# Optimization experiments

Hardware: AMD Instinct MI355X
Metric: run time of the kernel (lower is better)

Reference implementation:

```python
import jax, jax.numpy as jnp
import numpy as np
import math

B, S, D, H, N = 4, 2048, 1024, 8, 128  # batch, seq_len, d_model, n_heads, num_osc
ITERS = 10
DT = 0.1
PI = math.pi


def setup_inputs() -> dict:
    key = jax.random.key(0)
    ks = jax.random.split(key, 5)
    return {
        "x": jax.random.normal(ks[0], (B, S, D), jnp.float32),
        "mask": jnp.ones((B, S), jnp.int32),
        "W_phase": jax.random.normal(ks[1], (D, H * N), jnp.float32) / math.sqrt(D),
        "b_phase": jnp.zeros((H * N,), jnp.float32),
        "natural_freq": jax.random.normal(ks[2], (H, N), jnp.float32) * 0.1,
        "coupling": jnp.ones((H, 1, 1), jnp.float32),  # coupling_strength = 1.0
        "W_out": jax.random.normal(ks[3], (H * N, D), jnp.float32) / math.sqrt(H * N),
        "b_out": jnp.zeros((D,), jnp.float32),
    }


def reference(x, mask, W_phase, b_phase, natural_freq, coupling, W_out, b_out):
    # phases: [B, H, S, N]
    ph = (x @ W_phase + b_phase).reshape(B, S, H, N).transpose(0, 2, 1, 3)
    ph = jnp.tanh(ph) * PI
    m = mask.astype(ph.dtype)[:, None, :, None]  # [B,1,S,1] mask over j
    K = coupling.reshape(1, H, 1, 1)
    w = natural_freq.reshape(1, H, 1, N)

    def step(ph, _):
        s = jnp.sin(ph)
        c = jnp.cos(ph)
        # mean_j m_j * sin(theta_i - theta_j) = sin(th_i)*mean(m*cos) - cos(th_i)*mean(m*sin)
        ms = (m * s).mean(axis=2, keepdims=True)  # [B,H,1,N]
        mc = (m * c).mean(axis=2, keepdims=True)
        dtheta = w + K * (s * mc - c * ms)
        ph2 = jnp.mod(ph + DT * dtheta + PI, 2 * PI) - PI
        return ph2, None

    ph, _ = jax.lax.scan(step, ph, None, length=ITERS)
    # from_phase; dropout is identity in eval mode
    y = ph.transpose(0, 2, 1, 3).reshape(B, S, H * N) @ W_out + b_out
    return y
```

## Files before the change

### kernel.cpp

```cpp
#include <hip/hip_runtime.h>
#include <math.h>

#define S_ 2048
#define D_ 1024
#define HN_ 1024
#define B_ 4
#define M_ 8192
#define K1_ 3072
#define K3_ 1024
#define ITERS_ 10
#define DT_ 0.1f
#define PI_ 3.14159265358979323846f
#define TWOPI_ 6.28318530717958647692f
#define INV2PI_ 0.15915494309189533577f
#define SCALE_ 4096.0f
#define INVSC2_ (1.0f / 16777216.0f)

typedef __attribute__((ext_vector_type(8))) _Float16 f16x8;
typedef __attribute__((ext_vector_type(4))) float f32x4;

__device__ ushort g_xs [(size_t)M_ * K1_];
__device__ ushort g_WpT[(size_t)HN_ * K1_];
__device__ float  g_ph [(size_t)B_ * HN_ * S_];
__device__ ushort g_phh[(size_t)B_ * HN_ * S_];
__device__ ushort g_phT[(size_t)M_ * HN_];
__device__ ushort g_WoT[(size_t)D_ * HN_];

__device__ __forceinline__ ushort f2h(float f) {
    union { _Float16 h; ushort u; } v; v.h = (_Float16)f; return v.u;
}
__device__ __forceinline__ void split2s(float x, ushort& A, ushort& Bc) {
    const float xs = x * SCALE_;
    union { _Float16 h; ushort u; } va, vb;
    va.h = (_Float16)xs;
    const float r = xs - (float)va.h;
    vb.h = (_Float16)r;
    A = va.u; Bc = vb.u;
}
__device__ __forceinline__ void gload16(const void* g, void* l) {
    __builtin_amdgcn_global_load_lds(
        (const __attribute__((address_space(1))) void*)g,
        (__attribute__((address_space(3))) void*)l, 16, 0, 0);
}
__device__ __forceinline__ int pack2(ushort a, ushort b) {
    return (int)(unsigned)a | ((int)(unsigned)b << 16);
}

__global__ __launch_bounds__(256) void split_x(const float* __restrict__ X) {
    const int idx = blockIdx.x * 256 + threadIdx.x;
    const float4 v = ((const float4*)X)[idx];
    const int m  = idx >> 8;
    const int k4 = (idx & 255) * 4;
    ushort a[4], b[4];
    split2s(v.x, a[0], b[0]);
    split2s(v.y, a[1], b[1]);
    split2s(v.z, a[2], b[2]);
    split2s(v.w, a[3], b[3]);
    ushort* row = g_xs + (size_t)m * K1_ + k4;
    int2 oa; oa.x = pack2(a[0], a[1]); oa.y = pack2(a[2], a[3]);
    int2 ob; ob.x = pack2(b[0], b[1]); ob.y = pack2(b[2], b[3]);
    *(int2*)(row)        = oa;
    *(int2*)(row + 1024) = oa;
    *(int2*)(row + 2048) = ob;
}

__global__ __launch_bounds__(256) void splitT_Wp(const float* __restrict__ Wp) {
    __shared__ float t[64][68];
    const int k0 = blockIdx.x * 64;
    const int n0 = blockIdx.y * 64;
    const int r = threadIdx.x >> 2;
    const int c = (threadIdx.x & 3) * 16;
    const float* src = Wp + (size_t)(k0 + r) * HN_ + n0 + c;
    #pragma unroll
    for (int q = 0; q < 4; ++q)
        *(float4*)&t[r][c + 4 * q] = ((const float4*)src)[q];
    __syncthreads();
    ushort ha[16], hb[16];
    #pragma unroll
    for (int j = 0; j < 16; ++j)
        split2s(t[c + j][r], ha[j], hb[j]);
    int4 a0, a1, b0, b1;
    a0.x = pack2(ha[0], ha[1]);   a0.y = pack2(ha[2], ha[3]);
    a0.z = pack2(ha[4], ha[5]);   a0.w = pack2(ha[6], ha[7]);
    a1.x = pack2(ha[8], ha[9]);   a1.y = pack2(ha[10], ha[11]);
    a1.z = pack2(ha[12], ha[13]); a1.w = pack2(ha[14], ha[15]);
    b0.x = pack2(hb[0], hb[1]);   b0.y = pack2(hb[2], hb[3]);
    b0.z = pack2(hb[4], hb[5]);   b0.w = pack2(hb[6], hb[7]);
    b1.x = pack2(hb[8], hb[9]);   b1.y = pack2(hb[10], hb[11]);
    b1.z = pack2(hb[12], hb[13]); b1.w = pack2(hb[14], hb[15]);
    ushort* dst = g_WpT + (size_t)(n0 + r) * K1_ + k0 + c;
    *(int4*)(dst)            = a0; *(int4*)(dst + 8)        = a1;
    *(int4*)(dst + 1024)     = b0; *(int4*)(dst + 1032)     = b1;
    *(int4*)(dst + 2048)     = a0; *(int4*)(dst + 2056)     = a1;
}

__global__ __launch_bounds__(256) void castT_Wo(const float* __restrict__ Wo) {
    __shared__ float t[64][68];
    const int k0 = blockIdx.x * 64;
    const int n0 = blockIdx.y * 64;
    const int r = threadIdx.x >> 2;
    const int c = (threadIdx.x & 3) * 16;
    const float* src = Wo + (size_t)(k0 + r) * D_ + n0 + c;
    #pragma unroll
    for (int q = 0; q < 4; ++q)
        *(float4*)&t[r][c + 4 * q] = ((const float4*)src)[q];
    __syncthreads();
    ushort h[16];
    #pragma unroll
    for (int j = 0; j < 16; ++j) h[j] = f2h(t[c + j][r]);
    ushort* dst = g_WoT + (size_t)(n0 + r) * HN_ + k0 + c;
    int4 o0, o1;
    o0.x = pack2(h[0], h[1]);   o0.y = pack2(h[2], h[3]);
    o0.z = pack2(h[4], h[5]);   o0.w = pack2(h[6], h[7]);
    o1.x = pack2(h[8], h[9]);   o1.y = pack2(h[10], h[11]);
    o1.z = pack2(h[12], h[13]); o1.w = pack2(h[14], h[15]);
    *(int4*)dst = o0;
    *(int4*)(dst + 8) = o1;
}

template<int KDIM>
__device__ __forceinline__ void gemm_mainloop(const ushort* __restrict__ A,
                                              const ushort* __restrict__ Bm,
                                              ushort* lds,
                                              int m0, int n0, int wid, int l,
                                              int wm, int wn,
                                              f32x4 (&acc)[4][4]) {
    constexpr int NT = KDIM / 64;
    const int r8   = l >> 3;
    const int swzo = ((l & 7) * 16) ^ (r8 << 4);
    const char* gA = (const char*)(A + (size_t)m0 * KDIM);
    const char* gB = (const char*)(Bm + (size_t)n0 * KDIM);

    const int thr = (l & 15) * 128;
    const int f0  = (((l >> 4) * 16)      ^ ((l & 7) << 4));
    const int f1  = ((64 + (l >> 4) * 16) ^ ((l & 7) << 4));
    const char* pA0 = (const char*)lds + wm * 8192 + thr + f0;
    const char* pA1 = (const char*)lds + wm * 8192 + thr + f1;
    const char* pB0 = (const char*)lds + 16384 + wn * 8192 + thr + f0;
    const char* pB1 = (const char*)lds + 16384 + wn * 8192 + thr + f1;

    #define STAGE(T, BUF) do {                                                    \
        const size_t gb_ = (size_t)(T) * 128 + swzo;                              \
        char* lb_ = (char*)lds + (BUF) * 32768 + wid * 1024;                      \
        _Pragma("unroll")                                                         \
        for (int j_ = 0; j_ < 4; ++j_)                                            \
            gload16(gA + (size_t)(j_ * 32 + wid * 8 + r8) * (KDIM * 2) + gb_,     \
                    lb_ + j_ * 4096);                                             \
        _Pragma("unroll")                                                         \
        for (int j_ = 0; j_ < 4; ++j_)                                            \
            gload16(gB + (size_t)(j_ * 32 + wid * 8 + r8) * (KDIM * 2) + gb_,     \
                    lb_ + 16384 + j_ * 4096);                                     \
    } while (0)

    STAGE(0, 0);

    #pragma unroll 2
    for (int t = 0; t < NT; ++t) {
        __builtin_amdgcn_sched_barrier(0);
        __builtin_amdgcn_s_barrier();
        __builtin_amdgcn_sched_barrier(0);
        if (t + 1 < NT) {
            STAGE(t + 1, (t + 1) & 1);
            asm volatile("s_waitcnt vmcnt(8)" ::: "memory");
        } else {
            asm volatile("s_waitcnt vmcnt(0)" ::: "memory");
        }
        __builtin_amdgcn_sched_barrier(0);
        __builtin_amdgcn_s_barrier();
        __builtin_amdgcn_sched_barrier(0);

        const int bo = (t & 1) << 15;
        f16x8 Aa[4][2], Bb[4][2];
        #pragma unroll
        for (int i = 0; i < 4; ++i) {
            Aa[i][0] = *(const f16x8*)(pA0 + bo + i * 2048);
            Aa[i][1] = *(const f16x8*)(pA1 + bo + i * 2048);
        }
        #pragma unroll
        for (int j = 0; j < 4; ++j) {
            Bb[j][0] = *(const f16x8*)(pB0 + bo + j * 2048);
            Bb[j][1] = *(const f16x8*)(pB1 + bo + j * 2048);
        }
        __builtin_amdgcn_s_setprio(1);
        #pragma unroll
        for (int ks = 0; ks < 2; ++ks)
            #pragma unroll
            for (int i = 0; i < 4; ++i)
                #pragma unroll
                for (int j = 0; j < 4; ++j)
                    acc[i][j] = __builtin_amdgcn_mfma_f32_16x16x32_f16(
                        Aa[i][ks], Bb[j][ks], acc[i][j], 0, 0, 0);
        __builtin_amdgcn_s_setprio(0);
    }
    #undef STAGE
}

__device__ __forceinline__ void tile_map(int bid, int& m0, int& n0) {
    const int xcd = bid & 7;
    const int idx = bid >> 3;
    m0 = (xcd * 8 + (idx >> 3)) * 128;
    n0 = (idx & 7) * 128;
}

__global__ __launch_bounds__(256) void gemm1(const float* __restrict__ bias) {
    __shared__ ushort lds[2 * 16384];
    const int tid = threadIdx.x;
    const int wid = tid >> 6, l = tid & 63;
    int m0, n0;
    tile_map(blockIdx.x, m0, n0);
    const int wm = wid >> 1, wn = wid & 1;

    f32x4 acc[4][4];
    #pragma unroll
    for (int i = 0; i < 4; ++i)
        #pragma unroll
        for (int j = 0; j < 4; ++j) acc[i][j] = (f32x4){0.f, 0.f, 0.f, 0.f};

    gemm_mainloop<K1_>(g_xs, g_WpT, lds, m0, n0, wid, l, wm, wn, acc);

    const int r4 = (l >> 4) * 4;
    const int cn = l & 15;
    #pragma unroll
    for (int i = 0; i < 4; ++i) {
        const int mg = m0 + wm * 64 + i * 16 + r4;
        const int bidx = mg >> 11;
        const int sg = mg & 2047;
        #pragma unroll
        for (int jj = 0; jj < 4; ++jj) {
            const int ng = n0 + wn * 64 + jj * 16 + cn;
            const float bb = bias[ng];
            float4 o;
            o.x = PI_ * tanhf(fmaf(acc[i][jj][0], INVSC2_, bb));
            o.y = PI_ * tanhf(fmaf(acc[i][jj][1], INVSC2_, bb));
            o.z = PI_ * tanhf(fmaf(acc[i][jj][2], INVSC2_, bb));
            o.w = PI_ * tanhf(fmaf(acc[i][jj][3], INVSC2_, bb));
            *(float4*)(g_ph + ((size_t)bidx * HN_ + ng) * S_ + sg) = o;
        }
    }
}

__global__ __launch_bounds__(256) void gemm3(const float* __restrict__ bias,
                                             float* __restrict__ Y) {
    __shared__ ushort lds[2 * 16384];
    const int tid = threadIdx.x;
    const int wid = tid >> 6, l = tid & 63;
    int m0, n0;
    tile_map(blockIdx.x, m0, n0);
    const int wm = wid >> 1, wn = wid & 1;

    f32x4 acc[4][4];
    #pragma unroll
    for (int i = 0; i < 4; ++i)
        #pragma unroll
        for (int j = 0; j < 4; ++j) acc[i][j] = (f32x4){0.f, 0.f, 0.f, 0.f};

    gemm_mainloop<K3_>(g_phT, g_WoT, lds, m0, n0, wid, l, wm, wn, acc);

    const int r4 = (l >> 4) * 4;
    const int cn = l & 15;
    #pragma unroll
    for (int i = 0; i < 4; ++i) {
        const int mg = m0 + wm * 64 + i * 16 + r4;
        #pragma unroll
        for (int jj = 0; jj < 4; ++jj) {
            const int ng = n0 + wn * 64 + jj * 16 + cn;
            const float bb = bias[ng];
            #pragma unroll
            for (int r = 0; r < 4; ++r)
                Y[(size_t)(mg + r) * D_ + ng] = acc[i][jj][r] + bb;
        }
    }
}

__global__ __launch_bounds__(256) void kuramoto(const int* __restrict__ mask,
                                                const float* __restrict__ natf,
                                                const float* __restrict__ coup) {
    const int wave = blockIdx.x * 4 + (threadIdx.x >> 6);
    const int lane = threadIdx.x & 63;
    const int b = wave >> 10;
    const int hn = wave & 1023;
    const int h = hn >> 7;

    const float wf = natf[hn];
    const float K = coup[h];

    const float* base = g_ph + ((size_t)b * HN_ + hn) * S_;

    float ph[32];
    #pragma unroll
    for (int i = 0; i < 8; ++i) {
        float4 v = *(const float4*)(base + i * 256 + lane * 4);
        ph[4 * i + 0] = v.x; ph[4 * i + 1] = v.y;
        ph[4 * i + 2] = v.z; ph[4 * i + 3] = v.w;
    }

    const int* mb = mask + b * S_;
    unsigned mbits = 0;
    #pragma unroll
    for (int i = 0; i < 8; ++i) {
        int4 mv = *(const int4*)(mb + i * 256 + lane * 4);
        mbits |= (mv.x != 0 ? 1u : 0u) << (4 * i + 0);
        mbits |= (mv.y != 0 ? 1u : 0u) << (4 * i + 1);
        mbits |= (mv.z != 0 ? 1u : 0u) << (4 * i + 2);
        mbits |= (mv.w != 0 ? 1u : 0u) << (4 * i + 3);
    }

    for (int it = 0; it < ITERS_; ++it) {
        float s[32], c[32];
        float ls = 0.f, lc = 0.f;
        #pragma unroll
        for (int i = 0; i < 32; ++i) {
            s[i] = __sinf(ph[i]);
            c[i] = __cosf(ph[i]);
            const float mf = (float)((mbits >> i) & 1u);
            ls = fmaf(mf, s[i], ls);
            lc = fmaf(mf, c[i], lc);
        }
        #pragma unroll
        for (int off = 32; off; off >>= 1) {
            ls += __shfl_xor(ls, off);
            lc += __shfl_xor(lc, off);
        }
        const float ms = ls * (1.f / 2048.f);
        const float mc = lc * (1.f / 2048.f);
        #pragma unroll
        for (int i = 0; i < 32; ++i) {
            const float dth = fmaf(K, fmaf(s[i], mc, -c[i] * ms), wf);
            float t = fmaf(DT_, dth, ph[i]) + PI_;
            t -= TWOPI_ * floorf(t * INV2PI_);
            ph[i] = t - PI_;
        }
    }

    ushort* ob = g_phh + ((size_t)b * HN_ + hn) * S_;
    #pragma unroll
    for (int i = 0; i < 8; ++i) {
        ushort4 o;
        o.x = f2h(ph[4 * i + 0]); o.y = f2h(ph[4 * i + 1]);
        o.z = f2h(ph[4 * i + 2]); o.w = f2h(ph[4 * i + 3]);
        *(ushort4*)(ob + i * 256 + lane * 4) = o;
    }
}

__global__ __launch_bounds__(256) void transpose_ph() {
    __shared__ ushort t[64][72];
    const int b = blockIdx.z;
    const int h0 = blockIdx.y * 64;
    const int s0 = blockIdx.x * 64;
    const int r = threadIdx.x >> 2;
    const int c = (threadIdx.x & 3) * 16;
    const ushort* src = g_phh + ((size_t)b * HN_ + h0 + r) * S_ + s0 + c;
    *(int4*)&t[r][c] = *(const int4*)src;
    *(int4*)&t[r][c + 8] = *(const int4*)(src + 8);
    __syncthreads();
    ushort o[16];
    #pragma unroll
    for (int j = 0; j < 16; ++j) o[j] = t[c + j][r];
    ushort* dst = g_phT + ((size_t)(b * S_ + s0 + r)) * HN_ + h0 + c;
    int4 o0, o1;
    o0.x = pack2(o[0], o[1]);   o0.y = pack2(o[2], o[3]);
    o0.z = pack2(o[4], o[5]);   o0.w = pack2(o[6], o[7]);
    o1.x = pack2(o[8], o[9]);   o1.y = pack2(o[10], o[11]);
    o1.z = pack2(o[12], o[13]); o1.w = pack2(o[14], o[15]);
    *(int4*)dst = o0;
    *(int4*)(dst + 8) = o1;
}

extern "C" void kernel_launch(void* const* d_in, const int* in_sizes, int n_in,
                              void* d_out, int out_size, void* d_ws, size_t ws_size,
                              hipStream_t stream) {
    const float* x    = (const float*)d_in[0];
    const int*   mask = (const int*)d_in[1];
    const float* Wp   = (const float*)d_in[2];
    const float* bp   = (const float*)d_in[3];
    const float* natf = (const float*)d_in[4];
    const float* coup = (const float*)d_in[5];
    const float* Wo   = (const float*)d_in[6];
    const float* bo   = (const float*)d_in[7];
    float* y = (float*)d_out;

    split_x  <<<dim3(8192),         256, 0, stream>>>(x);
    splitT_Wp<<<dim3(16, 16),       256, 0, stream>>>(Wp);
    castT_Wo <<<dim3(16, 16),       256, 0, stream>>>(Wo);
    gemm1    <<<dim3(512),          256, 0, stream>>>(bp);
    kuramoto <<<dim3(1024),         256, 0, stream>>>(mask, natf, coup);
    transpose_ph<<<dim3(32, 16, 4), 256, 0, stream>>>();
    gemm3    <<<dim3(512),          256, 0, stream>>>(bo, y);
}
```

Baseline: 168.4 us.

## Use 8 waves per GEMM block with 64x32 warp tiles

The two fp16 MFMA GEMMs now launch 512 threads per 128x128 block instead of 256. Waves are laid out 2x4, each computing a 64x32 sub-tile, and each wave issues 4 global-to-LDS loads per stage instead of 8, with the vmcnt wait adjusted to match. The aim is more waves per CU to hide latency and fewer accumulator registers per wave. The cost is more LDS reads per MFMA, because B fragments are reused across fewer columns, and more barrier participants per block.

```diff
diff --git a/kernel.cpp b/kernel.cpp
--- a/kernel.cpp
+++ b/kernel.cpp
@@ -124,32 +124,27 @@
                                               ushort* lds,
                                               int m0, int n0, int wid, int l,
                                               int wm, int wn,
-                                              f32x4 (&acc)[4][4]) {
+                                              f32x4 (&acc)[4][2]) {
     constexpr int NT = KDIM / 64;
     const int r8   = l >> 3;
     const int swzo = ((l & 7) * 16) ^ (r8 << 4);
     const char* gA = (const char*)(A + (size_t)m0 * KDIM);
     const char* gB = (const char*)(Bm + (size_t)n0 * KDIM);
 
-    const int thr = (l & 15) * 128;
-    const int f0  = (((l >> 4) * 16)      ^ ((l & 7) << 4));
-    const int f1  = ((64 + (l >> 4) * 16) ^ ((l & 7) << 4));
-    const char* pA0 = (const char*)lds + wm * 8192 + thr + f0;
-    const char* pA1 = (const char*)lds + wm * 8192 + thr + f1;
-    const char* pB0 = (const char*)lds + 16384 + wn * 8192 + thr + f0;
-    const char* pB1 = (const char*)lds + 16384 + wn * 8192 + thr + f1;
+    const int l15 = l & 15;
+    const int xk  = (l15 & 7) << 4;
+    const int sl0 = (((l >> 4) * 16)) ^ xk;
+    const int sl1 = (64 + ((l >> 4) * 16)) ^ xk;
+    const char* pA = (const char*)lds + (wm * 64 + l15) * 128;
+    const char* pB = (const char*)lds + 16384 + (wn * 32 + l15) * 128;
 
     #define STAGE(T, BUF) do {                                                    \
         const size_t gb_ = (size_t)(T) * 128 + swzo;                              \
-        char* lb_ = (char*)lds + (BUF) * 32768 + wid * 1024;                      \
-        _Pragma("unroll")                                                         \
-        for (int j_ = 0; j_ < 4; ++j_)                                            \
-            gload16(gA + (size_t)(j_ * 32 + wid * 8 + r8) * (KDIM * 2) + gb_,     \
-                    lb_ + j_ * 4096);                                             \
-        _Pragma("unroll")                                                         \
-        for (int j_ = 0; j_ < 4; ++j_)                                            \
-            gload16(gB + (size_t)(j_ * 32 + wid * 8 + r8) * (KDIM * 2) + gb_,     \
-                    lb_ + 16384 + j_ * 4096);                                     \
+        char* lb_ = (char*)lds + (BUF) * 32768 + wid * 2048;                      \
+        gload16(gA + (size_t)(wid * 16 + r8)     * (KDIM * 2) + gb_, lb_);        \
+        gload16(gA + (size_t)(wid * 16 + 8 + r8) * (KDIM * 2) + gb_, lb_ + 1024); \
+        gload16(gB + (size_t)(wid * 16 + r8)     * (KDIM * 2) + gb_, lb_ + 16384);\
+        gload16(gB + (size_t)(wid * 16 + 8 + r8) * (KDIM * 2) + gb_, lb_ + 16384 + 1024); \
     } while (0)
 
     STAGE(0, 0);
@@ -161,7 +156,7 @@
         __builtin_amdgcn_sched_barrier(0);
         if (t + 1 < NT) {
             STAGE(t + 1, (t + 1) & 1);
-            asm volatile("s_waitcnt vmcnt(8)" ::: "memory");
+            asm volatile("s_waitcnt vmcnt(4)" ::: "memory");
         } else {
             asm volatile("s_waitcnt vmcnt(0)" ::: "memory");
         }
@@ -170,16 +165,16 @@
         __builtin_amdgcn_sched_barrier(0);
 
         const int bo = (t & 1) << 15;
-        f16x8 Aa[4][2], Bb[4][2];
+        f16x8 Aa[4][2], Bb[2][2];
         #pragma unroll
         for (int i = 0; i < 4; ++i) {
-            Aa[i][0] = *(const f16x8*)(pA0 + bo + i * 2048);
-            Aa[i][1] = *(const f16x8*)(pA1 + bo + i * 2048);
-        }
-        #pragma unroll
-        for (int j = 0; j < 4; ++j) {
-            Bb[j][0] = *(const f16x8*)(pB0 + bo + j * 2048);
-            Bb[j][1] = *(const f16x8*)(pB1 + bo + j * 2048);
+            Aa[i][0] = *(const f16x8*)(pA + bo + i * 2048 + sl0);
+            Aa[i][1] = *(const f16x8*)(pA + bo + i * 2048 + sl1);
+        }
+        #pragma unroll
+        for (int j = 0; j < 2; ++j) {
+            Bb[j][0] = *(const f16x8*)(pB + bo + j * 2048 + sl0);
+            Bb[j][1] = *(const f16x8*)(pB + bo + j * 2048 + sl1);
         }
         __builtin_amdgcn_s_setprio(1);
         #pragma unroll
@@ -187,7 +182,7 @@
             #pragma unroll
             for (int i = 0; i < 4; ++i)
                 #pragma unroll
-                for (int j = 0; j < 4; ++j)
+                for (int j = 0; j < 2; ++j)
                     acc[i][j] = __builtin_amdgcn_mfma_f32_16x16x32_f16(
                         Aa[i][ks], Bb[j][ks], acc[i][j], 0, 0, 0);
         __builtin_amdgcn_s_setprio(0);
@@ -202,19 +197,19 @@
     n0 = (idx & 7) * 128;
 }
 
-__global__ __launch_bounds__(256) void gemm1(const float* __restrict__ bias) {
+__global__ __launch_bounds__(512, 4) void gemm1(const float* __restrict__ bias) {
     __shared__ ushort lds[2 * 16384];
     const int tid = threadIdx.x;
     const int wid = tid >> 6, l = tid & 63;
     int m0, n0;
     tile_map(blockIdx.x, m0, n0);
-    const int wm = wid >> 1, wn = wid & 1;
-
-    f32x4 acc[4][4];
+    const int wm = wid >> 2, wn = wid & 3;
+
+    f32x4 acc[4][2];
     #pragma unroll
     for (int i = 0; i < 4; ++i)
         #pragma unroll
-        for (int j = 0; j < 4; ++j) acc[i][j] = (f32x4){0.f, 0.f, 0.f, 0.f};
+        for (int j = 0; j < 2; ++j) acc[i][j] = (f32x4){0.f, 0.f, 0.f, 0.f};
 
     gemm_mainloop<K1_>(g_xs, g_WpT, lds, m0, n0, wid, l, wm, wn, acc);
 
@@ -226,8 +221,8 @@
         const int bidx = mg >> 11;
         const int sg = mg & 2047;
         #pragma unroll
-        for (int jj = 0; jj < 4; ++jj) {
-            const int ng = n0 + wn * 64 + jj * 16 + cn;
+        for (int jj = 0; jj < 2; ++jj) {
+            const int ng = n0 + wn * 32 + jj * 16 + cn;
             const float bb = bias[ng];
             float4 o;
             o.x = PI_ * tanhf(fmaf(acc[i][jj][0], INVSC2_, bb));
@@ -239,20 +234,20 @@
     }
 }
 
-__global__ __launch_bounds__(256) void gemm3(const float* __restrict__ bias,
-                                             float* __restrict__ Y) {
+__global__ __launch_bounds__(512, 4) void gemm3(const float* __restrict__ bias,
+                                                float* __restrict__ Y) {
     __shared__ ushort lds[2 * 16384];
     const int tid = threadIdx.x;
     const int wid = tid >> 6, l = tid & 63;
     int m0, n0;
     tile_map(blockIdx.x, m0, n0);
-    const int wm = wid >> 1, wn = wid & 1;
-
-    f32x4 acc[4][4];
+    const int wm = wid >> 2, wn = wid & 3;
+
+    f32x4 acc[4][2];
     #pragma unroll
     for (int i = 0; i < 4; ++i)
         #pragma unroll
-        for (int j = 0; j < 4; ++j) acc[i][j] = (f32x4){0.f, 0.f, 0.f, 0.f};
+        for (int j = 0; j < 2; ++j) acc[i][j] = (f32x4){0.f, 0.f, 0.f, 0.f};
 
     gemm_mainloop<K3_>(g_phT, g_WoT, lds, m0, n0, wid, l, wm, wn, acc);
 
@@ -262,8 +257,8 @@
     for (int i = 0; i < 4; ++i) {
         const int mg = m0 + wm * 64 + i * 16 + r4;
         #pragma unroll
-        for (int jj = 0; jj < 4; ++jj) {
-            const int ng = n0 + wn * 64 + jj * 16 + cn;
+        for (int jj = 0; jj < 2; ++jj) {
+            const int ng = n0 + wn * 32 + jj * 16 + cn;
             const float bb = bias[ng];
             #pragma unroll
             for (int r = 0; r < 4; ++r)
@@ -382,8 +377,8 @@
     split_x  <<<dim3(8192),         256, 0, stream>>>(x);
     splitT_Wp<<<dim3(16, 16),       256, 0, stream>>>(Wp);
     castT_Wo <<<dim3(16, 16),       256, 0, stream>>>(Wo);
-    gemm1    <<<dim3(512),          256, 0, stream>>>(bp);
+    gemm1    <<<dim3(512),          512, 0, stream>>>(bp);
     kuramoto <<<dim3(1024),         256, 0, stream>>>(mask, natf, coup);
     transpose_ph<<<dim3(32, 16, 4), 256, 0, stream>>>();
-    gemm3    <<<dim3(512),          256, 0, stream>>>(bo, y);
-}
+    gemm3    <<<dim3(512),          512, 0, stream>>>(bo, y);
+}
```

Result: no change. 166.2 us (-1.3%).

## Stop storing duplicated split-fp16 copies; index hi/lo halves virtually in GEMM

Applied to the files above, without the earlier changes.

The split-precision GEMM previously materialised a 3K-wide operand (hi, hi, lo for x and hi, lo, hi for W) in global memory. Now only hi and lo halves are stored (2K wide), and the mainloop maps k-tiles onto the right halves via offset macros, so the duplicated segment is never written. The K-tile shrinks from 64 to 32 with a smaller LDS footprint and a launch bound of 4 blocks per SM to raise occupancy. The trade-off is more loop iterations and barriers per tile and more complex address arithmetic.

```diff
diff --git a/kernel.cpp b/kernel.cpp
--- a/kernel.cpp
+++ b/kernel.cpp
@@ -6,8 +6,6 @@
 #define HN_ 1024
 #define B_ 4
 #define M_ 8192
-#define K1_ 3072
-#define K3_ 1024
 #define ITERS_ 10
 #define DT_ 0.1f
 #define PI_ 3.14159265358979323846f
@@ -19,12 +17,12 @@
 typedef __attribute__((ext_vector_type(8))) _Float16 f16x8;
 typedef __attribute__((ext_vector_type(4))) float f32x4;
 
-__device__ ushort g_xs [(size_t)M_ * K1_];
-__device__ ushort g_WpT[(size_t)HN_ * K1_];
-__device__ float  g_ph [(size_t)B_ * HN_ * S_];
-__device__ ushort g_phh[(size_t)B_ * HN_ * S_];
-__device__ ushort g_phT[(size_t)M_ * HN_];
-__device__ ushort g_WoT[(size_t)D_ * HN_];
+__device__ __align__(16) ushort g_xs [(size_t)M_ * 2048];
+__device__ __align__(16) ushort g_WpT[(size_t)HN_ * 2048];
+__device__ __align__(16) ushort g_WoT[(size_t)D_ * 1024];
+__device__ __align__(16) float  g_ph [(size_t)B_ * HN_ * S_];
+__device__ __align__(16) ushort g_phh[(size_t)B_ * HN_ * S_];
+__device__ __align__(16) ushort g_phT[(size_t)M_ * HN_];
 
 __device__ __forceinline__ ushort f2h(float f) {
     union { _Float16 h; ushort u; } v; v.h = (_Float16)f; return v.u;
@@ -56,12 +54,11 @@
     split2s(v.y, a[1], b[1]);
     split2s(v.z, a[2], b[2]);
     split2s(v.w, a[3], b[3]);
-    ushort* row = g_xs + (size_t)m * K1_ + k4;
+    ushort* row = g_xs + (size_t)m * 2048 + k4;
     int2 oa; oa.x = pack2(a[0], a[1]); oa.y = pack2(a[2], a[3]);
     int2 ob; ob.x = pack2(b[0], b[1]); ob.y = pack2(b[2], b[3]);
     *(int2*)(row)        = oa;
-    *(int2*)(row + 1024) = oa;
-    *(int2*)(row + 2048) = ob;
+    *(int2*)(row + 1024) = ob;
 }
 
 __global__ __launch_bounds__(256) void splitT_Wp(const float* __restrict__ Wp) {
@@ -88,10 +85,9 @@
     b0.z = pack2(hb[4], hb[5]);   b0.w = pack2(hb[6], hb[7]);
     b1.x = pack2(hb[8], hb[9]);   b1.y = pack2(hb[10], hb[11]);
     b1.z = pack2(hb[12], hb[13]); b1.w = pack2(hb[14], hb[15]);
-    ushort* dst = g_WpT + (size_t)(n0 + r) * K1_ + k0 + c;
-    *(int4*)(dst)            = a0; *(int4*)(dst + 8)        = a1;
-    *(int4*)(dst + 1024)     = b0; *(int4*)(dst + 1032)     = b1;
-    *(int4*)(dst + 2048)     = a0; *(int4*)(dst + 2056)     = a1;
+    ushort* dst = g_WpT + (size_t)(n0 + r) * 2048 + k0 + c;
+    *(int4*)(dst)        = a0; *(int4*)(dst + 8)    = a1;
+    *(int4*)(dst + 1024) = b0; *(int4*)(dst + 1032) = b1;
 }
 
 __global__ __launch_bounds__(256) void castT_Wo(const float* __restrict__ Wo) {
@@ -108,7 +104,7 @@
     ushort h[16];
     #pragma unroll
     for (int j = 0; j < 16; ++j) h[j] = f2h(t[c + j][r]);
-    ushort* dst = g_WoT + (size_t)(n0 + r) * HN_ + k0 + c;
+    ushort* dst = g_WoT + (size_t)(n0 + r) * 1024 + k0 + c;
     int4 o0, o1;
     o0.x = pack2(h[0], h[1]);   o0.y = pack2(h[2], h[3]);
     o0.z = pack2(h[4], h[5]);   o0.w = pack2(h[6], h[7]);
@@ -118,81 +114,70 @@
     *(int4*)(dst + 8) = o1;
 }
 
-template<int KDIM>
+template<int NT, int SPLIT>
 __device__ __forceinline__ void gemm_mainloop(const ushort* __restrict__ A,
                                               const ushort* __restrict__ Bm,
                                               ushort* lds,
-                                              int m0, int n0, int wid, int l,
-                                              int wm, int wn,
+                                              int m0, int n0, int tid,
                                               f32x4 (&acc)[4][4]) {
-    constexpr int NT = KDIM / 64;
-    const int r8   = l >> 3;
-    const int swzo = ((l & 7) * 16) ^ (r8 << 4);
-    const char* gA = (const char*)(A + (size_t)m0 * KDIM);
-    const char* gB = (const char*)(Bm + (size_t)n0 * KDIM);
-
-    const int thr = (l & 15) * 128;
-    const int f0  = (((l >> 4) * 16)      ^ ((l & 7) << 4));
-    const int f1  = ((64 + (l >> 4) * 16) ^ ((l & 7) << 4));
-    const char* pA0 = (const char*)lds + wm * 8192 + thr + f0;
-    const char* pA1 = (const char*)lds + wm * 8192 + thr + f1;
-    const char* pB0 = (const char*)lds + 16384 + wn * 8192 + thr + f0;
-    const char* pB1 = (const char*)lds + 16384 + wn * 8192 + thr + f1;
+    constexpr int KROW = SPLIT ? 2048 : 1024;
+    const int l   = tid & 63, wid = tid >> 6;
+    const int wm  = wid >> 1, wn = wid & 1;
+    const int l15 = l & 15, h = l >> 4;
+    const int row4 = tid >> 2;
+    const int soff = ((tid & 3) ^ (row4 & 3)) << 4;
+    const char* gA = (const char*)(A + (size_t)m0 * KROW);
+    const char* gB = (const char*)(Bm + (size_t)n0 * KROW);
+    const int rdA = (wm * 64 + l15) * 64 + ((h ^ (l15 & 3)) << 4);
+    const int rdB = 8192 + (wn * 64 + l15) * 64 + ((h ^ (l15 & 3)) << 4);
+
+    #define AOFF(T) ((SPLIT && (T) >= 64) ? 2048 + ((T) - 64) * 64 : ((T) & 31) * 64)
+    #define BOFF(T) (SPLIT ? ((T) < 32 ? (T) * 64 : ((T) < 64 ? 2048 + ((T) - 32) * 64 \
+                                                              : ((T) - 64) * 64)) : (T) * 64)
 
     #define STAGE(T, BUF) do {                                                    \
-        const size_t gb_ = (size_t)(T) * 128 + swzo;                              \
-        char* lb_ = (char*)lds + (BUF) * 32768 + wid * 1024;                      \
-        _Pragma("unroll")                                                         \
-        for (int j_ = 0; j_ < 4; ++j_)                                            \
-            gload16(gA + (size_t)(j_ * 32 + wid * 8 + r8) * (KDIM * 2) + gb_,     \
-                    lb_ + j_ * 4096);                                             \
-        _Pragma("unroll")                                                         \
-        for (int j_ = 0; j_ < 4; ++j_)                                            \
-            gload16(gB + (size_t)(j_ * 32 + wid * 8 + r8) * (KDIM * 2) + gb_,     \
-                    lb_ + 16384 + j_ * 4096);                                     \
+        const int ao_ = AOFF(T), bo_ = BOFF(T);                                   \
+        char* lb_ = (char*)lds + (BUF) * 16384;                                   \
+        gload16(gA + (size_t)(row4)      * (KROW * 2) + ao_ + soff, lb_ + tid * 16);          \
+        gload16(gA + (size_t)(row4 + 64) * (KROW * 2) + ao_ + soff, lb_ + 4096 + tid * 16);   \
+        gload16(gB + (size_t)(row4)      * (KROW * 2) + bo_ + soff, lb_ + 8192 + tid * 16);   \
+        gload16(gB + (size_t)(row4 + 64) * (KROW * 2) + bo_ + soff, lb_ + 12288 + tid * 16);  \
     } while (0)
+
+    #define SB __builtin_amdgcn_sched_barrier(0)
 
     STAGE(0, 0);
 
     #pragma unroll 2
     for (int t = 0; t < NT; ++t) {
-        __builtin_amdgcn_sched_barrier(0);
-        __builtin_amdgcn_s_barrier();
-        __builtin_amdgcn_sched_barrier(0);
+        SB; __builtin_amdgcn_s_barrier(); SB;
         if (t + 1 < NT) {
             STAGE(t + 1, (t + 1) & 1);
-            asm volatile("s_waitcnt vmcnt(8)" ::: "memory");
+            asm volatile("s_waitcnt vmcnt(4)" ::: "memory");
         } else {
             asm volatile("s_waitcnt vmcnt(0)" ::: "memory");
         }
-        __builtin_amdgcn_sched_barrier(0);
-        __builtin_amdgcn_s_barrier();
-        __builtin_amdgcn_sched_barrier(0);
-
-        const int bo = (t & 1) << 15;
-        f16x8 Aa[4][2], Bb[4][2];
-        #pragma unroll
-        for (int i = 0; i < 4; ++i) {
-            Aa[i][0] = *(const f16x8*)(pA0 + bo + i * 2048);
-            Aa[i][1] = *(const f16x8*)(pA1 + bo + i * 2048);
-        }
-        #pragma unroll
-        for (int j = 0; j < 4; ++j) {
-            Bb[j][0] = *(const f16x8*)(pB0 + bo + j * 2048);
-            Bb[j][1] = *(const f16x8*)(pB1 + bo + j * 2048);
-        }
+        SB; __builtin_amdgcn_s_barrier(); SB;
+
+        const char* bb = (const char*)lds + (t & 1) * 16384;
+        f16x8 Aa[4], Bb[4];
+        #pragma unroll
+        for (int i = 0; i < 4; ++i) Aa[i] = *(const f16x8*)(bb + rdA + i * 1024);
+        #pragma unroll
+        for (int j = 0; j < 4; ++j) Bb[j] = *(const f16x8*)(bb + rdB + j * 1024);
         __builtin_amdgcn_s_setprio(1);
         #pragma unroll
-        for (int ks = 0; ks < 2; ++ks)
+        for (int i = 0; i < 4; ++i)
             #pragma unroll
-            for (int i = 0; i < 4; ++i)
-                #pragma unroll
-                for (int j = 0; j < 4; ++j)
-                    acc[i][j] = __builtin_amdgcn_mfma_f32_16x16x32_f16(
-                        Aa[i][ks], Bb[j][ks], acc[i][j], 0, 0, 0);
+            for (int j = 0; j < 4; ++j)
+                acc[i][j] = __builtin_amdgcn_mfma_f32_16x16x32_f16(
+                    Aa[i], Bb[j], acc[i][j], 0, 0, 0);
         __builtin_amdgcn_s_setprio(0);
     }
     #undef STAGE
+    #undef SB
+    #undef AOFF
+    #undef BOFF
 }
 
 __device__ __forceinline__ void tile_map(int bid, int& m0, int& n0) {
@@ -202,12 +187,12 @@
     n0 = (idx & 7) * 128;
 }
 
-__global__ __launch_bounds__(256) void gemm1(const float* __restrict__ bias) {
-    __shared__ ushort lds[2 * 16384];
+__global__ __launch_bounds__(256, 4) void gemm1(const float* __restrict__ bias) {
+    __shared__ ushort lds[2 * 8192];
     const int tid = threadIdx.x;
-    const int wid = tid >> 6, l = tid & 63;
     int m0, n0;
     tile_map(blockIdx.x, m0, n0);
+    const int wid = tid >> 6, l = tid & 63;
     const int wm = wid >> 1, wn = wid & 1;
 
     f32x4 acc[4][4];
@@ -216,7 +201,7 @@
         #pragma unroll
         for (int j = 0; j < 4; ++j) acc[i][j] = (f32x4){0.f, 0.f, 0.f, 0.f};
 
-    gemm_mainloop<K1_>(g_xs, g_WpT, lds, m0, n0, wid, l, wm, wn, acc);
+    gemm_mainloop<96, 1>(g_xs, g_WpT, lds, m0, n0, tid, acc);
 
     const int r4 = (l >> 4) * 4;
     const int cn = l & 15;
@@ -239,13 +224,13 @@
     }
 }
 
-__global__ __launch_bounds__(256) void gemm3(const float* __restrict__ bias,
-                                             float* __restrict__ Y) {
-    __shared__ ushort lds[2 * 16384];
+__global__ __launch_bounds__(256, 4) void gemm3(const float* __restrict__ bias,
+                                                float* __restrict__ Y) {
+    __shared__ ushort lds[2 * 8192];
     const int tid = threadIdx.x;
-    const int wid = tid >> 6, l = tid & 63;
     int m0, n0;
     tile_map(blockIdx.x, m0, n0);
+    const int wid = tid >> 6, l = tid & 63;
     const int wm = wid >> 1, wn = wid & 1;
 
     f32x4 acc[4][4];
@@ -254,7 +239,7 @@
         #pragma unroll
         for (int j = 0; j < 4; ++j) acc[i][j] = (f32x4){0.f, 0.f, 0.f, 0.f};
 
-    gemm_mainloop<K3_>(g_phT, g_WoT, lds, m0, n0, wid, l, wm, wn, acc);
+    gemm_mainloop<32, 0>(g_phT, g_WoT, lds, m0, n0, tid, acc);
 
     const int r4 = (l >> 4) * 4;
     const int cn = l & 15;
```

Measured after the change: 192.6 us. 1.14x slower.
